# Kernel optimization log

Measured on AMD Instinct MI355X. Metric: run time of the kernel, lower is better.

The kernel has to match this reference:

```python
import jax, jax.numpy as jnp
import numpy as np

N_FEATURES = 512
N_LAYERS = 128
BATCH = 2048
PI = np.pi


def setup_inputs() -> dict:
    key = jax.random.key(0)
    k0, k1, k2, k3, k4 = jax.random.split(key, 5)
    nA = N_FEATURES // 2            # angles per A layer (even pairs)
    nB = (N_FEATURES - 1) // 2      # angles per B layer (odd pairs)
    LB = N_LAYERS // 2
    LA = N_LAYERS - LB              # equal when N_LAYERS even
    return {
        "cmplx": jax.random.normal(k0, (BATCH, N_FEATURES, 2), dtype=jnp.float32),
        "angleA0": jax.random.uniform(k1, (LA, nA), jnp.float32, -PI, PI),
        "angleA1": jax.random.uniform(k2, (LA, nA), jnp.float32, -PI, PI),
        "angleB0": jax.random.uniform(k3, (LB, nB), jnp.float32, -PI, PI),
        "angleB1": jax.random.uniform(k4, (LB, nB), jnp.float32, -PI, PI),
        "omega": jnp.zeros((N_FEATURES,), jnp.float32),
    }


def _mzi(a, b, ang0, ang1):
    # MZI = DC . PS(ang1) . DC . PS(ang0) acting on mode pair (a, b)
    # U = 1/2 [[e^{i phi}(e^{i th}-1),    i(e^{i th}+1)   ],
    #          [i e^{i phi}(e^{i th}+1),  (1 - e^{i th})  ]]
    ephi = jnp.exp(1j * ang0)
    eth = jnp.exp(1j * ang1)
    t = 0.5 * (eth - 1.0)
    u = 0.5 * (eth + 1.0)
    na = ephi * t * a + 1j * u * b
    nb = 1j * ephi * u * a - t * b
    return na, nb


def _layer_A(x, a0, a1):
    # pairs (0,1),(2,3),...
    a = x[:, 0::2]
    b = x[:, 1::2]
    na, nb = _mzi(a, b, a0, a1)
    return jnp.stack([na, nb], axis=-1).reshape(x.shape)


def _layer_B(x, b0, b1):
    # pairs (1,2),(3,4),...; endpoints 0 and N-1 pass through (N even)
    N = x.shape[1]
    a = x[:, 1:N - 1:2]
    b = x[:, 2:N:2]
    na, nb = _mzi(a, b, b0, b1)
    mid = jnp.stack([na, nb], axis=-1).reshape(x.shape[0], N - 2)
    return jnp.concatenate([x[:, :1], mid, x[:, -1:]], axis=1)


def reference(cmplx, angleA0, angleA1, angleB0, angleB1, omega):
    x = cmplx[..., 0] + 1j * cmplx[..., 1]   # [B, N] complex64

    def step(x, angs):
        a0, a1, b0, b1 = angs
        x = _layer_A(x, a0, a1)
        x = _layer_B(x, b0, b1)
        return x, None

    x, _ = jax.lax.scan(step, x, (angleA0, angleA1, angleB0, angleB1))
    out = x * jnp.exp(1j * omega)            # complex diagonal phase
    return jnp.stack([out.real, out.imag], axis=-1)
```

## Files before the change

### kernel.cpp

```cpp
#include <hip/hip_runtime.h>

#define LSTEPS 64
#define NF 512
#define MB 2048
#define CSTRIDE 256

typedef __attribute__((ext_vector_type(8))) short bf16x8;
typedef __attribute__((ext_vector_type(4))) float f32x4;
typedef __attribute__((ext_vector_type(4))) int i32x4;

__device__ __forceinline__ float2 cmul(float2 a, float2 b) {
  return make_float2(fmaf(a.x, b.x, -(a.y * b.y)), fmaf(a.x, b.y, a.y * b.x));
}
__device__ __forceinline__ float2 cfma(float2 a, float2 b, float2 c) {
  return make_float2(fmaf(a.x, b.x, fmaf(-a.y, b.y, c.x)),
                     fmaf(a.x, b.y, fmaf(a.y, b.x, c.y)));
}
__device__ __forceinline__ unsigned short f2bf(float f) {
  union { float f; unsigned u; } v; v.f = f;
  unsigned r = v.u + 0x7FFF + ((v.u >> 16) & 1);
  return (unsigned short)(r >> 16);
}

__global__ __launch_bounds__(256) void prep_kernel(
    const float* __restrict__ a0, const float* __restrict__ a1,
    const float* __restrict__ b0, const float* __restrict__ b1,
    const float4* __restrict__ Xf,
    float4* __restrict__ cA, float4* __restrict__ cB,
    unsigned short* __restrict__ Xr, unsigned short* __restrict__ Xi)
{
  const int bid = blockIdx.x, tid = threadIdx.x;
  if (bid < 64) {
    const int l = bid;
    {
      float ang0 = a0[l * 256 + tid], ang1 = a1[l * 256 + tid];
      float se, ce, st, ct;
      sincosf(ang0, &se, &ce);
      sincosf(ang1, &st, &ct);
      float2 ephi = make_float2(ce, se);
      float2 tt = make_float2(0.5f * (ct - 1.0f), 0.5f * st);
      float2 uu = make_float2(0.5f * (ct + 1.0f), 0.5f * st);
      float2 C1 = cmul(ephi, tt);
      float2 C2 = make_float2(-uu.y, uu.x);
      float2 eu = cmul(ephi, uu);
      float2 C3 = make_float2(-eu.y, eu.x);
      float2 C4 = make_float2(-tt.x, -tt.y);
      float4* dst = cA + (size_t)(l * CSTRIDE + tid) * 2;
      dst[0] = make_float4(C1.x, C1.y, C2.x, C2.y);
      dst[1] = make_float4(C3.x, C3.y, C4.x, C4.y);
    }
    if (tid < 255) {
      float ang0 = b0[l * 255 + tid], ang1 = b1[l * 255 + tid];
      float se, ce, st, ct;
      sincosf(ang0, &se, &ce);
      sincosf(ang1, &st, &ct);
      float2 ephi = make_float2(ce, se);
      float2 tt = make_float2(0.5f * (ct - 1.0f), 0.5f * st);
      float2 uu = make_float2(0.5f * (ct + 1.0f), 0.5f * st);
      float2 C1 = cmul(ephi, tt);
      float2 C2 = make_float2(-uu.y, uu.x);
      float2 eu = cmul(ephi, uu);
      float2 C3 = make_float2(-eu.y, eu.x);
      float2 C4 = make_float2(-tt.x, -tt.y);
      float4* dst = cB + (size_t)(l * CSTRIDE + tid) * 2;
      dst[0] = make_float4(C1.x, C1.y, C2.x, C2.y);
      dst[1] = make_float4(C3.x, C3.y, C4.x, C4.y);
    } else {
      float4* dst = cB + (size_t)(l * CSTRIDE + 255) * 2;
      dst[0] = make_float4(0.f, 0.f, 0.f, 0.f);
      dst[1] = make_float4(0.f, 0.f, 0.f, 0.f);
    }
  } else {
    const int qi = (bid - 64) * 256 + tid;
    float4 v0 = Xf[(size_t)qi * 2];
    float4 v1 = Xf[(size_t)qi * 2 + 1];
    ushort4 r, im;
    r.x = f2bf(v0.x); im.x = f2bf(v0.y);
    r.y = f2bf(v0.z); im.y = f2bf(v0.w);
    r.z = f2bf(v1.x); im.z = f2bf(v1.y);
    r.w = f2bf(v1.z); im.w = f2bf(v1.w);
    *(ushort4*)(Xr + (size_t)qi * 4) = r;
    *(ushort4*)(Xi + (size_t)qi * 4) = im;
  }
}

struct MZS { float2 a0, b0, a1, b1; };

__device__ __forceinline__ void mzi_apply(const float4& k0, const float4& k1,
                                          float2& a, float2& b) {
  float2 c1 = make_float2(k0.x, k0.y), c2 = make_float2(k0.z, k0.w);
  float2 c3 = make_float2(k1.x, k1.y), c4 = make_float2(k1.z, k1.w);
  float2 na = cfma(c2, b, cmul(c1, a));
  float2 nb = cfma(c4, b, cmul(c3, a));
  a = na; b = nb;
}
__device__ __forceinline__ float2 mzi_bnd(const float4& k0, const float4& k1,
                                          float2& a, float2 b, bool en) {
  float2 d1 = make_float2(k0.x, k0.y), d2 = make_float2(k0.z, k0.w);
  float2 d3 = make_float2(k1.x, k1.y), d4 = make_float2(k1.z, k1.w);
  float2 na = cfma(d2, b, cmul(d1, a));
  float2 nb = cfma(d4, b, cmul(d3, a));
  if (en) a = na;
  return en ? nb : make_float2(0.f, 0.f);
}

__device__ __forceinline__ void load_bank(float4 (&K)[8],
    const float4* __restrict__ cA, const float4* __restrict__ cB, int l, int q0)
{
  const float4* pa = cA + (size_t)l * (CSTRIDE * 2) + (size_t)q0 * 2;
  const float4* pb = cB + (size_t)l * (CSTRIDE * 2) + (size_t)q0 * 2;
  K[0] = pa[0]; K[1] = pa[1]; K[2] = pa[2]; K[3] = pa[3];
  K[4] = pb[0]; K[5] = pb[1]; K[6] = pb[2]; K[7] = pb[3];
}

__device__ __forceinline__ void step_state(const float4 (&K)[8], int L, bool hasBnd,
                                           MZS& s)
{
  mzi_apply(K[0], K[1], s.a0, s.b0);
  mzi_apply(K[2], K[3], s.a1, s.b1);
  float xnx = __shfl_down(s.a0.x, 1);
  float xny = __shfl_down(s.a0.y, 1);
  float2 xn = (L == 63) ? make_float2(0.f, 0.f) : make_float2(xnx, xny);
  float2 nbo = mzi_bnd(K[6], K[7], s.b1, xn, hasBnd);
  mzi_apply(K[4], K[5], s.b0, s.a1);
  float px = __shfl_up(nbo.x, 1);
  float py = __shfl_up(nbo.y, 1);
  if (L > 0) s.a0 = make_float2(px, py);
}

__global__ __launch_bounds__(64) void mesh_kernel(
    const float4* __restrict__ cA, const float4* __restrict__ cB,
    unsigned short* __restrict__ Ur, unsigned short* __restrict__ Ui)
{
  const int bid = blockIdx.x;
  const int c = (bid & 7) * 32 + (bid >> 3);
  const int L = threadIdx.x;
  int ws = c - 63; ws = ws < 0 ? 0 : (ws > 128 ? 128 : ws);
  const int q0 = ws + 2 * L, q1 = q0 + 1;
  const bool hasBnd = (q1 < 255);

  MZS s0, s1;
  s0.a0 = make_float2((q0 == c) ? 1.f : 0.f, 0.f);
  s0.b0 = make_float2(0.f, 0.f);
  s0.a1 = make_float2((q1 == c) ? 1.f : 0.f, 0.f);
  s0.b1 = make_float2(0.f, 0.f);
  s1.a0 = make_float2(0.f, 0.f);
  s1.b0 = make_float2((q0 == c) ? 1.f : 0.f, 0.f);
  s1.a1 = make_float2(0.f, 0.f);
  s1.b1 = make_float2((q1 == c) ? 1.f : 0.f, 0.f);

  float4 K0[8], K1[8], K2[8];
  load_bank(K0, cA, cB, 0, q0);
  load_bank(K1, cA, cB, 1, q0);
  load_bank(K2, cA, cB, 2, q0);

#pragma unroll 1
  for (int l = 0; l < 63; l += 3) {
    step_state(K0, L, hasBnd, s0); step_state(K0, L, hasBnd, s1);
    load_bank(K0, cA, cB, (l + 3 < 64) ? l + 3 : 63, q0);
    step_state(K1, L, hasBnd, s0); step_state(K1, L, hasBnd, s1);
    load_bank(K1, cA, cB, (l + 4 < 64) ? l + 4 : 63, q0);
    step_state(K2, L, hasBnd, s0); step_state(K2, L, hasBnd, s1);
    load_bank(K2, cA, cB, (l + 5 < 64) ? l + 5 : 63, q0);
  }
  step_state(K0, L, hasBnd, s0); step_state(K0, L, hasBnd, s1);

  unsigned* Ur32 = (unsigned*)Ur;
  unsigned* Ui32 = (unsigned*)Ui;
  const int rows[4] = {2 * q0, 2 * q0 + 1, 2 * q1, 2 * q1 + 1};
  const float2 v0[4] = {s0.a0, s0.b0, s0.a1, s0.b1};
  const float2 v1[4] = {s1.a0, s1.b0, s1.a1, s1.b1};
#pragma unroll
  for (int e = 0; e < 4; ++e) {
    unsigned pr = (unsigned)f2bf(v0[e].x) | ((unsigned)f2bf(v1[e].x) << 16);
    unsigned pi = (unsigned)f2bf(v0[e].y) | ((unsigned)f2bf(v1[e].y) << 16);
    Ur32[(size_t)rows[e] * (NF / 2) + c] = pr;
    Ui32[(size_t)rows[e] * (NF / 2) + c] = pi;
  }
#pragma unroll
  for (int e = 0; e < 4; ++e) {
    const int row = (2 * ws + 256 + 4 * L + e) & 511;
    Ur32[(size_t)row * (NF / 2) + c] = 0u;
    Ui32[(size_t)row * (NF / 2) + c] = 0u;
  }
}

#define BMT 32
#define BNT 64
#define LDT 72

__global__ __launch_bounds__(256) void cgemm_kernel(
    const unsigned short* __restrict__ Xr, const unsigned short* __restrict__ Xi,
    const unsigned short* __restrict__ Ur, const unsigned short* __restrict__ Ui,
    const float* __restrict__ omega,
    float2* __restrict__ Y)
{
  __shared__ __align__(16) unsigned short Ars[BMT][LDT];
  __shared__ __align__(16) unsigned short Ais[BMT][LDT];
  __shared__ __align__(16) unsigned short Brs[BNT][LDT];
  __shared__ __align__(16) unsigned short Bis[BNT][LDT];

  const int tid = threadIdx.x;
  const int w = tid >> 6;
  const int wm = w & 1;
  const int wn = w >> 1;
  const int lane = tid & 63;
  const int bm = (blockIdx.x >> 3) * BMT;
  const int bn = (blockIdx.x & 7) * BNT;

  int klo = bn - 132; klo = klo < 0 ? 0 : klo; klo &= ~63;
  int khi = bn + 196; khi = khi > NF ? NF : khi; khi = (khi + 63) & ~63;

  f32x4 acc_r[2], acc_i[2];
#pragma unroll
  for (int nf = 0; nf < 2; ++nf) {
    acc_r[nf] = (f32x4){0.f, 0.f, 0.f, 0.f};
    acc_i[nf] = (f32x4){0.f, 0.f, 0.f, 0.f};
  }

  const int sar = tid >> 3, sak = (tid & 7) * 8;
  const int sbr = tid >> 2, sbk = (tid & 3) * 16;

  for (int k0 = klo; k0 < khi; k0 += 64) {
    const uint4* gar = (const uint4*)(Xr + (size_t)(bm + sar) * NF + k0 + sak);
    const uint4* gai = (const uint4*)(Xi + (size_t)(bm + sar) * NF + k0 + sak);
    const uint4* gbr = (const uint4*)(Ur + (size_t)(bn + sbr) * NF + k0 + sbk);
    const uint4* gbi = (const uint4*)(Ui + (size_t)(bn + sbr) * NF + k0 + sbk);
    uint4 ar = gar[0];
    uint4 ai = gai[0];
    uint4 br0 = gbr[0], br1 = gbr[1];
    uint4 bi0 = gbi[0], bi1 = gbi[1];

    if (k0 > klo) __syncthreads();

    *(uint4*)&Ars[sar][sak]     = ar;
    *(uint4*)&Ais[sar][sak]     = ai;
    *(uint4*)&Brs[sbr][sbk]     = br0;
    *(uint4*)&Brs[sbr][sbk + 8] = br1;
    *(uint4*)&Bis[sbr][sbk]     = bi0;
    *(uint4*)&Bis[sbr][sbk + 8] = bi1;

    __syncthreads();

#pragma unroll
    for (int kk = 0; kk < 2; ++kk) {
      const int ko = kk * 32 + (lane >> 4) * 8;
      bf16x8 afr = *(const bf16x8*)&Ars[wm * 16 + (lane & 15)][ko];
      bf16x8 afi = *(const bf16x8*)&Ais[wm * 16 + (lane & 15)][ko];
      i32x4 neg = (i32x4)afi ^ (int)0x80008000;
      bf16x8 afin = (bf16x8)neg;
#pragma unroll
      for (int nf = 0; nf < 2; ++nf) {
        bf16x8 bfr = *(const bf16x8*)&Brs[wn * 32 + nf * 16 + (lane & 15)][ko];
        bf16x8 bfi = *(const bf16x8*)&Bis[wn * 32 + nf * 16 + (lane & 15)][ko];
        acc_r[nf] = __builtin_amdgcn_mfma_f32_16x16x32_bf16(afr,  bfr, acc_r[nf], 0, 0, 0);
        acc_r[nf] = __builtin_amdgcn_mfma_f32_16x16x32_bf16(afin, bfi, acc_r[nf], 0, 0, 0);
        acc_i[nf] = __builtin_amdgcn_mfma_f32_16x16x32_bf16(afr,  bfi, acc_i[nf], 0, 0, 0);
        acc_i[nf] = __builtin_amdgcn_mfma_f32_16x16x32_bf16(afi,  bfr, acc_i[nf], 0, 0, 0);
      }
    }
  }

  const int dn0 = bn + wn * 32 + (lane & 15);
  const int dm0 = bm + wm * 16 + (lane >> 4) * 4;
#pragma unroll
  for (int nf = 0; nf < 2; ++nf) {
    const int n = dn0 + nf * 16;
    float sn, cn;
    sincosf(omega[n], &sn, &cn);
#pragma unroll
    for (int r = 0; r < 4; ++r) {
      float yr = acc_r[nf][r], yi = acc_i[nf][r];
      Y[(size_t)(dm0 + r) * NF + n] =
          make_float2(fmaf(yr, cn, -(yi * sn)), fmaf(yr, sn, yi * cn));
    }
  }
}

extern "C" void kernel_launch(void* const* d_in, const int* in_sizes, int n_in,
                              void* d_out, int out_size, void* d_ws, size_t ws_size,
                              hipStream_t stream) {
  const float* cmplx = (const float*)d_in[0];
  const float* a0    = (const float*)d_in[1];
  const float* a1    = (const float*)d_in[2];
  const float* b0    = (const float*)d_in[3];
  const float* b1    = (const float*)d_in[4];
  const float* omega = (const float*)d_in[5];

  size_t off = 0;
  float4* cA = (float4*)((char*)d_ws + off); off += (size_t)LSTEPS * CSTRIDE * 2 * sizeof(float4);
  float4* cB = (float4*)((char*)d_ws + off); off += (size_t)LSTEPS * CSTRIDE * 2 * sizeof(float4);
  unsigned short* Ur = (unsigned short*)((char*)d_ws + off); off += (size_t)NF * NF * 2;
  unsigned short* Ui = (unsigned short*)((char*)d_ws + off); off += (size_t)NF * NF * 2;
  unsigned short* Xr = (unsigned short*)((char*)d_ws + off); off += (size_t)MB * NF * 2;
  unsigned short* Xi = (unsigned short*)((char*)d_ws + off); off += (size_t)MB * NF * 2;

  prep_kernel<<<1088, 256, 0, stream>>>(a0, a1, b0, b1, (const float4*)cmplx,
                                        cA, cB, Xr, Xi);
  mesh_kernel<<<256, 64, 0, stream>>>(cA, cB, Ur, Ui);
  cgemm_kernel<<<(MB / BMT) * (NF / BNT), 256, 0, stream>>>(
      Xr, Xi, Ur, Ui, omega, (float2*)d_out);
}
```

Baseline: 50.14 us.

## Split mesh into eight chunks and combine via banded matrix product tree

The serial 64-step mesh propagation becomes eight independent 8-step chunk kernels (2048 blocks instead of 256), each emitting a chunk matrix plus its transpose. Three rounds of banded bf16 MFMA complex matrix products then combine the chunks pairwise into the full transfer matrix used by the final GEMM. This is meant to cut the long sequential latency of the single-wave mesh kernel and fill the GPU. In exchange it adds three kernel launches, much more workspace traffic, scattered transposed stores, and extra bf16 rounding at each product level, which may hurt accuracy.

```diff
diff --git a/kernel.cpp b/kernel.cpp
--- a/kernel.cpp
+++ b/kernel.cpp
@@ -4,6 +4,8 @@
 #define NF 512
 #define MB 2048
 #define CSTRIDE 256
+#define PL (NF * NF)
+#define LDT 72
 
 typedef __attribute__((ext_vector_type(8))) short bf16x8;
 typedef __attribute__((ext_vector_type(4))) float f32x4;
@@ -103,7 +105,6 @@
   if (en) a = na;
   return en ? nb : make_float2(0.f, 0.f);
 }
-
 __device__ __forceinline__ void load_bank(float4 (&K)[8],
     const float4* __restrict__ cA, const float4* __restrict__ cB, int l, int q0)
 {
@@ -112,7 +113,6 @@
   K[0] = pa[0]; K[1] = pa[1]; K[2] = pa[2]; K[3] = pa[3];
   K[4] = pb[0]; K[5] = pb[1]; K[6] = pb[2]; K[7] = pb[3];
 }
-
 __device__ __forceinline__ void step_state(const float4 (&K)[8], int L, bool hasBnd,
                                            MZS& s)
 {
@@ -128,12 +128,14 @@
   if (L > 0) s.a0 = make_float2(px, py);
 }
 
-__global__ __launch_bounds__(64) void mesh_kernel(
+__global__ __launch_bounds__(64) void chunk_mesh(
     const float4* __restrict__ cA, const float4* __restrict__ cB,
-    unsigned short* __restrict__ Ur, unsigned short* __restrict__ Ui)
+    unsigned short* __restrict__ Cbase)
 {
   const int bid = blockIdx.x;
-  const int c = (bid & 7) * 32 + (bid >> 3);
+  const int m = bid >> 8;
+  const int cb = bid & 255;
+  const int c = (cb & 7) * 32 + (cb >> 3);
   const int L = threadIdx.x;
   int ws = c - 63; ws = ws < 0 ? 0 : (ws > 128 ? 128 : ws);
   const int q0 = ws + 2 * L, q1 = q0 + 1;
@@ -149,24 +151,33 @@
   s1.a1 = make_float2(0.f, 0.f);
   s1.b1 = make_float2((q1 == c) ? 1.f : 0.f, 0.f);
 
+  const int l0 = m * 8;
   float4 K0[8], K1[8], K2[8];
-  load_bank(K0, cA, cB, 0, q0);
-  load_bank(K1, cA, cB, 1, q0);
-  load_bank(K2, cA, cB, 2, q0);
-
-#pragma unroll 1
-  for (int l = 0; l < 63; l += 3) {
-    step_state(K0, L, hasBnd, s0); step_state(K0, L, hasBnd, s1);
-    load_bank(K0, cA, cB, (l + 3 < 64) ? l + 3 : 63, q0);
-    step_state(K1, L, hasBnd, s0); step_state(K1, L, hasBnd, s1);
-    load_bank(K1, cA, cB, (l + 4 < 64) ? l + 4 : 63, q0);
-    step_state(K2, L, hasBnd, s0); step_state(K2, L, hasBnd, s1);
-    load_bank(K2, cA, cB, (l + 5 < 64) ? l + 5 : 63, q0);
-  }
+  load_bank(K0, cA, cB, l0 + 0, q0);
+  load_bank(K1, cA, cB, l0 + 1, q0);
+  load_bank(K2, cA, cB, l0 + 2, q0);
+
   step_state(K0, L, hasBnd, s0); step_state(K0, L, hasBnd, s1);
-
-  unsigned* Ur32 = (unsigned*)Ur;
-  unsigned* Ui32 = (unsigned*)Ui;
+  load_bank(K0, cA, cB, l0 + 3, q0);
+  step_state(K1, L, hasBnd, s0); step_state(K1, L, hasBnd, s1);
+  load_bank(K1, cA, cB, l0 + 4, q0);
+  step_state(K2, L, hasBnd, s0); step_state(K2, L, hasBnd, s1);
+  load_bank(K2, cA, cB, l0 + 5, q0);
+  step_state(K0, L, hasBnd, s0); step_state(K0, L, hasBnd, s1);
+  load_bank(K0, cA, cB, l0 + 6, q0);
+  step_state(K1, L, hasBnd, s0); step_state(K1, L, hasBnd, s1);
+  load_bank(K1, cA, cB, l0 + 7, q0);
+  step_state(K2, L, hasBnd, s0); step_state(K2, L, hasBnd, s1);
+  step_state(K0, L, hasBnd, s0); step_state(K0, L, hasBnd, s1);
+  step_state(K1, L, hasBnd, s0); step_state(K1, L, hasBnd, s1);
+
+  unsigned short* Cn_r = Cbase + (size_t)m * 4 * PL;
+  unsigned short* Cn_i = Cn_r + PL;
+  unsigned short* Ct_r = Cn_r + 2 * PL;
+  unsigned short* Ct_i = Cn_r + 3 * PL;
+  unsigned* nr32 = (unsigned*)Cn_r;
+  unsigned* ni32 = (unsigned*)Cn_i;
+
   const int rows[4] = {2 * q0, 2 * q0 + 1, 2 * q1, 2 * q1 + 1};
   const float2 v0[4] = {s0.a0, s0.b0, s0.a1, s0.b1};
   const float2 v1[4] = {s1.a0, s1.b0, s1.a1, s1.b1};
@@ -174,20 +185,141 @@
   for (int e = 0; e < 4; ++e) {
     unsigned pr = (unsigned)f2bf(v0[e].x) | ((unsigned)f2bf(v1[e].x) << 16);
     unsigned pi = (unsigned)f2bf(v0[e].y) | ((unsigned)f2bf(v1[e].y) << 16);
-    Ur32[(size_t)rows[e] * (NF / 2) + c] = pr;
-    Ui32[(size_t)rows[e] * (NF / 2) + c] = pi;
+    nr32[(size_t)rows[e] * (NF / 2) + c] = pr;
+    ni32[(size_t)rows[e] * (NF / 2) + c] = pi;
   }
 #pragma unroll
   for (int e = 0; e < 4; ++e) {
     const int row = (2 * ws + 256 + 4 * L + e) & 511;
-    Ur32[(size_t)row * (NF / 2) + c] = 0u;
-    Ui32[(size_t)row * (NF / 2) + c] = 0u;
-  }
-}
-
-#define BMT 32
-#define BNT 64
-#define LDT 72
+    nr32[(size_t)row * (NF / 2) + c] = 0u;
+    ni32[(size_t)row * (NF / 2) + c] = 0u;
+  }
+  const int j0 = 2 * c, j1 = 2 * c + 1;
+  const int i0 = 2 * q0;
+  *(ushort2*)&Ct_r[(size_t)j0 * NF + i0]     = make_ushort2(f2bf(v0[0].x), f2bf(v0[1].x));
+  *(ushort2*)&Ct_r[(size_t)j0 * NF + i0 + 2] = make_ushort2(f2bf(v0[2].x), f2bf(v0[3].x));
+  *(ushort2*)&Ct_i[(size_t)j0 * NF + i0]     = make_ushort2(f2bf(v0[0].y), f2bf(v0[1].y));
+  *(ushort2*)&Ct_i[(size_t)j0 * NF + i0 + 2] = make_ushort2(f2bf(v0[2].y), f2bf(v0[3].y));
+  *(ushort2*)&Ct_r[(size_t)j1 * NF + i0]     = make_ushort2(f2bf(v1[0].x), f2bf(v1[1].x));
+  *(ushort2*)&Ct_r[(size_t)j1 * NF + i0 + 2] = make_ushort2(f2bf(v1[2].x), f2bf(v1[3].x));
+  *(ushort2*)&Ct_i[(size_t)j1 * NF + i0]     = make_ushort2(f2bf(v1[0].y), f2bf(v1[1].y));
+  *(ushort2*)&Ct_i[(size_t)j1 * NF + i0 + 2] = make_ushort2(f2bf(v1[2].y), f2bf(v1[3].y));
+  const int iz = (2 * ws + 256 + 4 * L) & 511;
+  const int iz2 = (iz + 2) & 511;
+  const ushort2 zz = make_ushort2(0, 0);
+  *(ushort2*)&Ct_r[(size_t)j0 * NF + iz]  = zz;
+  *(ushort2*)&Ct_r[(size_t)j0 * NF + iz2] = zz;
+  *(ushort2*)&Ct_i[(size_t)j0 * NF + iz]  = zz;
+  *(ushort2*)&Ct_i[(size_t)j0 * NF + iz2] = zz;
+  *(ushort2*)&Ct_r[(size_t)j1 * NF + iz]  = zz;
+  *(ushort2*)&Ct_r[(size_t)j1 * NF + iz2] = zz;
+  *(ushort2*)&Ct_i[(size_t)j1 * NF + iz]  = zz;
+  *(ushort2*)&Ct_i[(size_t)j1 * NF + iz2] = zz;
+}
+
+__global__ __launch_bounds__(256) void prod_kernel(
+    const unsigned short* __restrict__ baseT,
+    const unsigned short* __restrict__ baseN,
+    unsigned short* __restrict__ baseW,
+    int zStrT, int zStrN, int hwA, int hwB)
+{
+  __shared__ __align__(16) unsigned short Ars[32][LDT];
+  __shared__ __align__(16) unsigned short Ais[32][LDT];
+  __shared__ __align__(16) unsigned short Brs[64][LDT];
+  __shared__ __align__(16) unsigned short Bis[64][LDT];
+
+  const int z = blockIdx.z;
+  const unsigned short* XT_r = baseT + (size_t)z * zStrT;
+  const unsigned short* XT_i = XT_r + PL;
+  const unsigned short* UN_r = baseN + (size_t)z * zStrN;
+  const unsigned short* UN_i = UN_r + PL;
+  unsigned short* Wnr = baseW + (size_t)z * 4 * PL;
+  unsigned short* Wni = Wnr + PL;
+  unsigned short* Wtr = Wnr + 2 * PL;
+  unsigned short* Wti = Wnr + 3 * PL;
+
+  const int tid = threadIdx.x;
+  const int w = tid >> 6, wm = w & 1, wn = w >> 1;
+  const int lane = tid & 63;
+  const int bm = blockIdx.x * 32;
+  const int bn = blockIdx.y * 64;
+
+  int klo = bn - hwA; { int t = bm - hwB; if (t > klo) klo = t; }
+  if (klo < 0) klo = 0; klo &= ~63;
+  int khi = bn + 64 + hwA; { int t = bm + 32 + hwB; if (t < khi) khi = t; }
+  if (khi > NF) khi = NF; khi = (khi + 63) & ~63;
+
+  f32x4 acc_r[2], acc_i[2];
+#pragma unroll
+  for (int nf = 0; nf < 2; ++nf) {
+    acc_r[nf] = (f32x4){0.f, 0.f, 0.f, 0.f};
+    acc_i[nf] = (f32x4){0.f, 0.f, 0.f, 0.f};
+  }
+  const int sar = tid >> 3, sak = (tid & 7) * 8;
+  const int sbr = tid >> 2, sbk = (tid & 3) * 16;
+
+  for (int k0 = klo; k0 < khi; k0 += 64) {
+    const uint4* gar = (const uint4*)(XT_r + (size_t)(bm + sar) * NF + k0 + sak);
+    const uint4* gai = (const uint4*)(XT_i + (size_t)(bm + sar) * NF + k0 + sak);
+    const uint4* gbr = (const uint4*)(UN_r + (size_t)(bn + sbr) * NF + k0 + sbk);
+    const uint4* gbi = (const uint4*)(UN_i + (size_t)(bn + sbr) * NF + k0 + sbk);
+    uint4 ar = gar[0];
+    uint4 ai = gai[0];
+    uint4 br0 = gbr[0], br1 = gbr[1];
+    uint4 bi0 = gbi[0], bi1 = gbi[1];
+
+    if (k0 > klo) __syncthreads();
+
+    *(uint4*)&Ars[sar][sak]     = ar;
+    *(uint4*)&Ais[sar][sak]     = ai;
+    *(uint4*)&Brs[sbr][sbk]     = br0;
+    *(uint4*)&Brs[sbr][sbk + 8] = br1;
+    *(uint4*)&Bis[sbr][sbk]     = bi0;
+    *(uint4*)&Bis[sbr][sbk + 8] = bi1;
+
+    __syncthreads();
+
+#pragma unroll
+    for (int kk = 0; kk < 2; ++kk) {
+      const int ko = kk * 32 + (lane >> 4) * 8;
+      bf16x8 afr = *(const bf16x8*)&Ars[wm * 16 + (lane & 15)][ko];
+      bf16x8 afi = *(const bf16x8*)&Ais[wm * 16 + (lane & 15)][ko];
+      i32x4 neg = (i32x4)afi ^ (int)0x80008000;
+      bf16x8 afin = (bf16x8)neg;
+#pragma unroll
+      for (int nf = 0; nf < 2; ++nf) {
+        bf16x8 bfr = *(const bf16x8*)&Brs[wn * 32 + nf * 16 + (lane & 15)][ko];
+        bf16x8 bfi = *(const bf16x8*)&Bis[wn * 32 + nf * 16 + (lane & 15)][ko];
+        acc_r[nf] = __builtin_amdgcn_mfma_f32_16x16x32_bf16(afr,  bfr, acc_r[nf], 0, 0, 0);
+        acc_r[nf] = __builtin_amdgcn_mfma_f32_16x16x32_bf16(afin, bfi, acc_r[nf], 0, 0, 0);
+        acc_i[nf] = __builtin_amdgcn_mfma_f32_16x16x32_bf16(afr,  bfi, acc_i[nf], 0, 0, 0);
+        acc_i[nf] = __builtin_amdgcn_mfma_f32_16x16x32_bf16(afi,  bfr, acc_i[nf], 0, 0, 0);
+      }
+    }
+  }
+
+  const int dn0 = bn + wn * 32 + (lane & 15);
+  const int dm0 = bm + wm * 16 + (lane >> 4) * 4;
+#pragma unroll
+  for (int nf = 0; nf < 2; ++nf) {
+    const int n = dn0 + nf * 16;
+    ushort4 pr, pi;
+    pr.x = f2bf(acc_r[nf][0]); pr.y = f2bf(acc_r[nf][1]);
+    pr.z = f2bf(acc_r[nf][2]); pr.w = f2bf(acc_r[nf][3]);
+    pi.x = f2bf(acc_i[nf][0]); pi.y = f2bf(acc_i[nf][1]);
+    pi.z = f2bf(acc_i[nf][2]); pi.w = f2bf(acc_i[nf][3]);
+    *(ushort4*)&Wnr[(size_t)n * NF + dm0] = pr;
+    *(ushort4*)&Wni[(size_t)n * NF + dm0] = pi;
+    Wtr[(size_t)(dm0 + 0) * NF + n] = pr.x;
+    Wtr[(size_t)(dm0 + 1) * NF + n] = pr.y;
+    Wtr[(size_t)(dm0 + 2) * NF + n] = pr.z;
+    Wtr[(size_t)(dm0 + 3) * NF + n] = pr.w;
+    Wti[(size_t)(dm0 + 0) * NF + n] = pi.x;
+    Wti[(size_t)(dm0 + 1) * NF + n] = pi.y;
+    Wti[(size_t)(dm0 + 2) * NF + n] = pi.z;
+    Wti[(size_t)(dm0 + 3) * NF + n] = pi.w;
+  }
+}
 
 __global__ __launch_bounds__(256) void cgemm_kernel(
     const unsigned short* __restrict__ Xr, const unsigned short* __restrict__ Xi,
@@ -195,21 +327,19 @@
     const float* __restrict__ omega,
     float2* __restrict__ Y)
 {
-  __shared__ __align__(16) unsigned short Ars[BMT][LDT];
-  __shared__ __align__(16) unsigned short Ais[BMT][LDT];
-  __shared__ __align__(16) unsigned short Brs[BNT][LDT];
-  __shared__ __align__(16) unsigned short Bis[BNT][LDT];
+  __shared__ __align__(16) unsigned short Ars[32][LDT];
+  __shared__ __align__(16) unsigned short Ais[32][LDT];
+  __shared__ __align__(16) unsigned short Brs[64][LDT];
+  __shared__ __align__(16) unsigned short Bis[64][LDT];
 
   const int tid = threadIdx.x;
-  const int w = tid >> 6;
-  const int wm = w & 1;
-  const int wn = w >> 1;
+  const int w = tid >> 6, wm = w & 1, wn = w >> 1;
   const int lane = tid & 63;
-  const int bm = (blockIdx.x >> 3) * BMT;
-  const int bn = (blockIdx.x & 7) * BNT;
-
-  int klo = bn - 132; klo = klo < 0 ? 0 : klo; klo &= ~63;
-  int khi = bn + 196; khi = khi > NF ? NF : khi; khi = (khi + 63) & ~63;
+  const int bm = (blockIdx.x >> 3) * 32;
+  const int bn = (blockIdx.x & 7) * 64;
+
+  int klo = bn - 136; if (klo < 0) klo = 0; klo &= ~63;
+  int khi = bn + 200; if (khi > NF) khi = NF; khi = (khi + 63) & ~63;
 
   f32x4 acc_r[2], acc_i[2];
 #pragma unroll
@@ -217,7 +347,6 @@
     acc_r[nf] = (f32x4){0.f, 0.f, 0.f, 0.f};
     acc_i[nf] = (f32x4){0.f, 0.f, 0.f, 0.f};
   }
-
   const int sar = tid >> 3, sak = (tid & 7) * 8;
   const int sbr = tid >> 2, sbk = (tid & 3) * 16;
 
@@ -290,14 +419,22 @@
   size_t off = 0;
   float4* cA = (float4*)((char*)d_ws + off); off += (size_t)LSTEPS * CSTRIDE * 2 * sizeof(float4);
   float4* cB = (float4*)((char*)d_ws + off); off += (size_t)LSTEPS * CSTRIDE * 2 * sizeof(float4);
-  unsigned short* Ur = (unsigned short*)((char*)d_ws + off); off += (size_t)NF * NF * 2;
-  unsigned short* Ui = (unsigned short*)((char*)d_ws + off); off += (size_t)NF * NF * 2;
   unsigned short* Xr = (unsigned short*)((char*)d_ws + off); off += (size_t)MB * NF * 2;
   unsigned short* Xi = (unsigned short*)((char*)d_ws + off); off += (size_t)MB * NF * 2;
+  unsigned short* Cb = (unsigned short*)((char*)d_ws + off); off += (size_t)8 * 4 * PL * 2;
+  unsigned short* W1 = (unsigned short*)((char*)d_ws + off); off += (size_t)4 * 4 * PL * 2;
+  unsigned short* W2 = (unsigned short*)((char*)d_ws + off); off += (size_t)2 * 4 * PL * 2;
+  unsigned short* Uu = (unsigned short*)((char*)d_ws + off); off += (size_t)1 * 4 * PL * 2;
 
   prep_kernel<<<1088, 256, 0, stream>>>(a0, a1, b0, b1, (const float4*)cmplx,
                                         cA, cB, Xr, Xi);
-  mesh_kernel<<<256, 64, 0, stream>>>(cA, cB, Ur, Ui);
-  cgemm_kernel<<<(MB / BMT) * (NF / BNT), 256, 0, stream>>>(
-      Xr, Xi, Ur, Ui, omega, (float2*)d_out);
-}
+  chunk_mesh<<<2048, 64, 0, stream>>>(cA, cB, Cb);
+  prod_kernel<<<dim3(16, 8, 4), 256, 0, stream>>>(
+      Cb + 2 * PL, Cb + 4 * PL, W1, 8 * PL, 8 * PL, 17, 17);
+  prod_kernel<<<dim3(16, 8, 2), 256, 0, stream>>>(
+      W1 + 2 * PL, W1 + 4 * PL, W2, 8 * PL, 8 * PL, 34, 34);
+  prod_kernel<<<dim3(16, 8, 1), 256, 0, stream>>>(
+      W2 + 2 * PL, W2 + 4 * PL, Uu, 8 * PL, 8 * PL, 68, 68);
+  cgemm_kernel<<<(MB / 32) * (NF / 64), 256, 0, stream>>>(
+      Xr, Xi, Uu, Uu + PL, omega, (float2*)d_out);
+}
```

After: 61.15 us. +21.9%, slower.
